# Kernel tuning notes

Measured on AMD Instinct MI355X. Metric: run time of the kernel, lower is better.

The kernel has to match this reference:

```python
import jax, jax.numpy as jnp
import numpy as np

B, N, D, H = 4, 4096, 1024, 16
HD = D // H  # 64
EPS_NORM = 1e-12  # F.normalize eps
EPS_LN = 1e-5     # layernorm eps


def setup_inputs() -> dict:
    key = jax.random.key(0)
    ks = jax.random.split(key, 9)
    s = 0.02
    return {
        "x": jax.random.normal(ks[0], (B, N, D), jnp.float32),
        "Wq": jax.random.normal(ks[1], (D, D), jnp.float32) * s,
        "Wk": jax.random.normal(ks[2], (D, D), jnp.float32) * s,
        "Wv": jax.random.normal(ks[3], (D, D), jnp.float32) * s,
        "Wf": jax.random.normal(ks[4], (H, D), jnp.float32) * s,
        "Wg1": jax.random.normal(ks[5], (HD, D), jnp.float32) * s,
        "Wg2": jax.random.normal(ks[6], (D, HD), jnp.float32) * s,
        "ln_w": jnp.ones((D,), jnp.float32),
        "Wo": jax.random.normal(ks[7], (D, D), jnp.float32) * s,
    }


def _silu(x):
    return x * jax.nn.sigmoid(x)


def _simple_gla(q, k, v, f):
    # q,k,v: [B,N,H,HD], f: [B,N,H] log-decay. Recurrence:
    #   S_t = exp(f_t) * S_{t-1} + k_t v_t^T ;  o_t = q_t^T S_t  (scale=1)
    qT = jnp.moveaxis(q, 1, 0)  # [N,B,H,HD]
    kT = jnp.moveaxis(k, 1, 0)
    vT = jnp.moveaxis(v, 1, 0)
    fT = jnp.moveaxis(f, 1, 0)  # [N,B,H]

    def step(S, inp):
        qt, kt, vt, ft = inp
        S = jnp.exp(ft)[..., None, None] * S + kt[..., :, None] * vt[..., None, :]
        o = jnp.einsum('bhk,bhkv->bhv', qt, S)
        return S, o

    S0 = jnp.zeros((q.shape[0], q.shape[2], q.shape[3], v.shape[3]), q.dtype)
    _, o = jax.lax.scan(step, S0, (qT, kT, vT, fT))
    return jnp.moveaxis(o, 0, 1)  # [B,N,H,HD]


def reference(x, Wq, Wk, Wv, Wf, Wg1, Wg2, ln_w, Wo):
    b, n, d = x.shape
    q = _silu(x @ Wq.T).reshape(b, n, H, HD)
    k = _silu(x @ Wk.T).reshape(b, n, H, HD)
    v = _silu(x @ Wv.T).reshape(b, n, H, HD)
    f = jax.nn.log_sigmoid(x @ Wf.T)  # [B,N,H] scalar per-head log decay
    # F.normalize(k, p=2, dim=-1)
    k = k / jnp.maximum(jnp.linalg.norm(k, axis=-1, keepdims=True), EPS_NORM)

    o = _simple_gla(q, k, v, f).reshape(b, n, d)

    # output gate: sigmoid(Linear(d->hd) -> Linear(hd->d))
    gate = jax.nn.sigmoid((x @ Wg1.T) @ Wg2.T)
    o = o * gate

    # layernorm without bias
    mu = jnp.mean(o, axis=-1, keepdims=True)
    xc = o - mu
    var = jnp.mean(xc * xc, axis=-1, keepdims=True)
    o = xc / jnp.sqrt(var + EPS_LN) * ln_w

    return o @ Wo.T
```

## Files before the change

kernel.cpp:

```cpp
#include <hip/hip_runtime.h>
#include <stdint.h>


#define NWIDE 3200

typedef __attribute__((ext_vector_type(4))) float f32x4;
typedef __attribute__((ext_vector_type(4))) unsigned short u16x4;
typedef __attribute__((ext_vector_type(8))) unsigned short u16x8;
typedef __attribute__((ext_vector_type(8))) __bf16 bf16x8;

__device__ __forceinline__ float bf2f(unsigned short u) {
    union { unsigned int i; float f; } c; c.i = ((unsigned int)u) << 16; return c.f;
}
__device__ __forceinline__ unsigned short f2bf(float f) {
    union { float f; unsigned int i; } c; c.f = f;
    return (unsigned short)((c.i + 0x7fffu + ((c.i >> 16) & 1u)) >> 16);
}
__device__ __forceinline__ float siluf(float x) { return x / (1.f + __expf(-x)); }
__device__ __forceinline__ float logsigf(float z) {
    return (z >= 0.f) ? -log1pf(__expf(-z)) : (z - log1pf(__expf(z)));
}
__device__ __forceinline__ f32x4 MFMA(bf16x8 a, bf16x8 b, f32x4 c) {
    return __builtin_amdgcn_mfma_f32_16x16x32_bf16(a, b, c, 0, 0, 0);
}
__device__ __forceinline__ void lds16(const void* g, void* l) {
    __builtin_amdgcn_global_load_lds(
        (const __attribute__((address_space(1))) unsigned int*)(uintptr_t)g,
        (__attribute__((address_space(3))) unsigned int*)(unsigned int)(uintptr_t)l,
        16, 0, 0);
}

__global__ __launch_bounds__(256)
void k_prep(const float* __restrict__ x, const float* __restrict__ Wq, const float* __restrict__ Wk,
            const float* __restrict__ Wv, const float* __restrict__ Wf, const float* __restrict__ Wg1,
            const float* __restrict__ Wg2, const float* __restrict__ lnw, const float* __restrict__ Wo,
            unsigned short* __restrict__ xb, unsigned short* __restrict__ Wcat,
            unsigned short* __restrict__ Wob, unsigned short* __restrict__ Wg2b,
            float* __restrict__ scol) {
    const int blk = blockIdx.x, t = threadIdx.x;
    if (blk < 16384) {
        const int i = blk * 256 + t;
        f32x4 v = ((const f32x4*)x)[i];
        u16x4 o;
#pragma unroll
        for (int e = 0; e < 4; e++) o[e] = f2bf(v[e]);
        ((u16x4*)xb)[i] = o;
    } else if (blk < 19584) {
        const int r = blk - 16384;
        const float* src = nullptr; int sr = r;
        if (r < 1024) { src = Wq; }
        else if (r < 2048) { src = Wk; sr = r - 1024; }
        else if (r < 3072) { src = Wv; sr = r - 2048; }
        else if (r < 3088) { src = Wf; sr = r - 3072; }
        else if (r < 3152) { src = Wg1; sr = r - 3088; }
        u16x4 o;
        if (src) {
            f32x4 v = *(const f32x4*)&src[(size_t)sr * 1024 + 4 * t];
#pragma unroll
            for (int e = 0; e < 4; e++) o[e] = f2bf(v[e]);
        } else {
            o[0] = 0; o[1] = 0; o[2] = 0; o[3] = 0;
        }
        *(u16x4*)&Wcat[(size_t)r * 1024 + 4 * t] = o;
    } else if (blk < 20608) {
        __shared__ float red[4];
        const int c = blk - 19584;
        f32x4 wv = *(const f32x4*)&Wo[(size_t)c * 1024 + 4 * t];
        f32x4 lv = *(const f32x4*)&lnw[4 * t];
        u16x4 o; float ps = 0.f;
#pragma unroll
        for (int e = 0; e < 4; e++) { o[e] = f2bf(wv[e] * lv[e]); ps += bf2f(o[e]); }
        *(u16x4*)&Wob[(size_t)c * 1024 + 4 * t] = o;
#pragma unroll
        for (int m = 1; m < 64; m <<= 1) ps += __shfl_xor(ps, m, 64);
        if ((t & 63) == 0) red[t >> 6] = ps;
        __syncthreads();
        if (t == 0) scol[c] = red[0] + red[1] + red[2] + red[3];
    } else {
        const int i = (blk - 20608) * 256 + t;
        f32x4 v = ((const f32x4*)Wg2)[i];
        u16x4 o;
#pragma unroll
        for (int e = 0; e < 4; e++) o[e] = f2bf(v[e]);
        ((u16x4*)Wg2b)[i] = o;
    }
}

template <int MODE>
__global__ __launch_bounds__(256)
void k_gemm(const unsigned short* __restrict__ A, const unsigned short* __restrict__ Bw,
            void* __restrict__ outp, float* __restrict__ zbuf,
            const float* __restrict__ stats, const float* __restrict__ scol,
            int M, int N, int K, int ldOut) {
    __shared__ __align__(16) unsigned short As[128 * 64];
    __shared__ __align__(16) unsigned short Bs[128 * 64];
    const int tid = threadIdx.x;
    const int w = tid >> 6, lane = tid & 63;
    const int m0 = blockIdx.x * 128, n0 = blockIdx.y * 128;
    const int fr = lane & 15, fg = lane >> 4;
    const int wr = w >> 1, wc = w & 1;
    const int srow = lane >> 3;
    const int schunk = (lane & 7) ^ (srow & 7);
    f32x4 acc[4][4] = {};
    const int kc = K >> 6;
    for (int kt = 0; kt < kc; ++kt) {
        const int k0 = kt << 6;
        __syncthreads();
#pragma unroll
        for (int q = 0; q < 4; q++) {
            const int rr = 32 * w + 8 * q;
            lds16(A + (size_t)(m0 + rr + srow) * K + k0 + schunk * 8, &As[rr * 64]);
            lds16(Bw + (size_t)(n0 + rr + srow) * K + k0 + schunk * 8, &Bs[rr * 64]);
        }
        __syncthreads();
        bf16x8 av[4][2], bv[4][2];
#pragma unroll
        for (int i = 0; i < 4; i++)
#pragma unroll
            for (int ks = 0; ks < 2; ks++) {
                const int row = 64 * wr + 16 * i + fr;
                av[i][ks] = *(const bf16x8*)&As[row * 64 + (((ks * 4 + fg) ^ (row & 7)) << 3)];
            }
#pragma unroll
        for (int j = 0; j < 4; j++)
#pragma unroll
            for (int ks = 0; ks < 2; ks++) {
                const int row = 64 * wc + 16 * j + fr;
                bv[j][ks] = *(const bf16x8*)&Bs[row * 64 + (((ks * 4 + fg) ^ (row & 7)) << 3)];
            }
#pragma unroll
        for (int i = 0; i < 4; i++)
#pragma unroll
            for (int j = 0; j < 4; j++)
#pragma unroll
                for (int ks = 0; ks < 2; ks++)
                    acc[i][j] = MFMA(av[i][ks], bv[j][ks], acc[i][j]);
    }
    const int nb = n0 + 64 * wc;
    if (MODE == 1) {
        float* O = (float*)outp;
        float sj[4];
#pragma unroll
        for (int j = 0; j < 4; j++) sj[j] = scol[nb + 16 * j + fr];
#pragma unroll
        for (int i = 0; i < 4; i++)
#pragma unroll
            for (int r = 0; r < 4; r++) {
                const int gr = m0 + 64 * wr + 16 * i + 4 * fg + r;
                const float mu = stats[gr * 2], rs = stats[gr * 2 + 1];
#pragma unroll
                for (int j = 0; j < 4; j++)
                    O[(size_t)gr * ldOut + nb + 16 * j + fr] = rs * (acc[i][j][r] - mu * sj[j]);
            }
        return;
    }
    unsigned short* Y = (unsigned short*)outp;
    if (nb >= 3072) {
#pragma unroll
        for (int i = 0; i < 4; i++)
#pragma unroll
            for (int j = 0; j < 4; j++) {
                const int gc = nb + 16 * j + fr;
#pragma unroll
                for (int r = 0; r < 4; r++) {
                    const int gr = m0 + 64 * wr + 16 * i + 4 * fg + r;
                    const float v = acc[i][j][r];
                    if (gc < 3088) {
                        if (gc >= 3072) zbuf[gr * 16 + (gc - 3072)] = v;
                    } else if (gc < 3152) {
                        Y[(size_t)gr * ldOut + gc] = f2bf(v);
                    }
                }
            }
    } else {
#pragma unroll
        for (int i = 0; i < 4; i++)
#pragma unroll
            for (int j = 0; j < 4; j++) {
                const int gc = nb + 16 * j + fr;
#pragma unroll
                for (int r = 0; r < 4; r++)
                    Y[(size_t)(m0 + 64 * wr + 16 * i + 4 * fg + r) * ldOut + gc] = f2bf(acc[i][j][r]);
            }
    }
}

__global__ __launch_bounds__(256)
void k_chunk_kv(const unsigned short* __restrict__ Y, const float* __restrict__ zbuf,
                float* __restrict__ cbuf, unsigned short* __restrict__ St) {
    __shared__ __align__(16) unsigned short Kt[64 * 72];
    __shared__ __align__(16) unsigned short Vt[64 * 72];
    __shared__ float cs[64];
    const int cid = blockIdx.x, tid = threadIdx.x;
    const int bh = cid >> 6, ic = cid & 63;
    const int b = bh >> 4, h = bh & 15;
    if (tid < 64) {
        float v = logsigf(zbuf[(size_t)(b * 4096 + ic * 64 + tid) * 16 + h]);
#pragma unroll
        for (int off = 1; off < 64; off <<= 1) {
            float u = __shfl_up(v, (unsigned)off, 64);
            if (tid >= off) v += u;
        }
        cs[tid] = v;
        cbuf[(size_t)cid * 64 + tid] = v;
    }
    __syncthreads();
    const int s = tid >> 2, c0 = (tid & 3) << 4;
    const float wdec = __expf(cs[63] - cs[s]);
    const size_t rowg = (size_t)(b * 4096 + ic * 64 + s) * NWIDE;
    u16x8 k0v = *(const u16x8*)&Y[rowg + 1024 + h * 64 + c0];
    u16x8 k1v = *(const u16x8*)&Y[rowg + 1024 + h * 64 + c0 + 8];
    u16x8 v0v = *(const u16x8*)&Y[rowg + 2048 + h * 64 + c0];
    u16x8 v1v = *(const u16x8*)&Y[rowg + 2048 + h * 64 + c0 + 8];
    float kf[16]; float ss = 0.f;
#pragma unroll
    for (int e = 0; e < 8; e++) { kf[e] = siluf(bf2f(k0v[e])); ss += kf[e] * kf[e]; }
#pragma unroll
    for (int e = 0; e < 8; e++) { kf[8 + e] = siluf(bf2f(k1v[e])); ss += kf[8 + e] * kf[8 + e]; }
    ss += __shfl_xor(ss, 1, 64);
    ss += __shfl_xor(ss, 2, 64);
    const float sc = wdec / fmaxf(sqrtf(ss), 1e-12f);
#pragma unroll
    for (int e = 0; e < 8; e++) {
        Kt[(c0 + e) * 72 + s] = f2bf(kf[e] * sc);
        Kt[(c0 + 8 + e) * 72 + s] = f2bf(kf[8 + e] * sc);
        Vt[(c0 + e) * 72 + s] = f2bf(siluf(bf2f(v0v[e])));
        Vt[(c0 + 8 + e) * 72 + s] = f2bf(siluf(bf2f(v1v[e])));
    }
    __syncthreads();
    const int w = tid >> 6, lane = tid & 63;
    const int fr = lane & 15, fg = lane >> 4;
    f32x4 acc[4] = {};
#pragma unroll
    for (int ks = 0; ks < 2; ks++) {
        bf16x8 a = *(const bf16x8*)&Kt[(16 * w + fr) * 72 + ks * 32 + fg * 8];
#pragma unroll
        for (int j = 0; j < 4; j++)
            acc[j] = MFMA(a, *(const bf16x8*)&Vt[(16 * j + fr) * 72 + ks * 32 + fg * 8], acc[j]);
    }
    unsigned short* outp = St + (size_t)cid * 4096;
#pragma unroll
    for (int j = 0; j < 4; j++)
#pragma unroll
        for (int r = 0; r < 4; r++)
            outp[(16 * w + 4 * fg + r) * 64 + 16 * j + fr] = f2bf(acc[j][r]);
}

__global__ void k_scan(unsigned short* __restrict__ St, const float* __restrict__ cbuf) {
    const int bh = blockIdx.x >> 4;
    const int e = ((blockIdx.x & 15) << 8) + threadIdx.x;
    float S = 0.f;
    const size_t base = (size_t)bh * 64 * 4096 + e;
    for (int i = 0; i < 64; i++) {
        const float d = __expf(cbuf[(bh * 64 + i) * 64 + 63]);
        const float m = bf2f(St[base + (size_t)i * 4096]);
        St[base + (size_t)i * 4096] = f2bf(S);
        S = d * S + m;
    }
}

__global__ __launch_bounds__(256)
void k_chunk_out(const unsigned short* __restrict__ Y, const float* __restrict__ cbuf,
                 const unsigned short* __restrict__ St, const unsigned short* __restrict__ Wg2b,
                 unsigned short* __restrict__ og) {
    __shared__ __align__(16) unsigned short Qs[64 * 72];
    __shared__ __align__(16) unsigned short Ks[64 * 72];
    __shared__ __align__(16) unsigned short Vt[64 * 72];
    __shared__ __align__(16) unsigned short S0[64 * 72];
    __shared__ __align__(16) unsigned short G1[64 * 72];
    __shared__ __align__(16) unsigned short W2[64 * 72];
    __shared__ __align__(16) unsigned short Pl[4 * 16 * 72];
    __shared__ float cs[64];
    const int cid = blockIdx.x, tid = threadIdx.x;
    const int bh = cid >> 6, ic = cid & 63;
    const int b = bh >> 4, h = bh & 15;
    if (tid < 64) cs[tid] = cbuf[(size_t)cid * 64 + tid];
    const int s = tid >> 2, c0 = (tid & 3) << 4;
    const size_t rowg = (size_t)(b * 4096 + ic * 64 + s) * NWIDE;
    {
        u16x8 q0 = *(const u16x8*)&Y[rowg + h * 64 + c0];
        u16x8 q1 = *(const u16x8*)&Y[rowg + h * 64 + c0 + 8];
        u16x8 o0, o1;
#pragma unroll
        for (int e = 0; e < 8; e++) { o0[e] = f2bf(siluf(bf2f(q0[e]))); o1[e] = f2bf(siluf(bf2f(q1[e]))); }
        *(u16x8*)&Qs[s * 72 + c0] = o0;
        *(u16x8*)&Qs[s * 72 + c0 + 8] = o1;
    }
    {
        u16x8 k0v = *(const u16x8*)&Y[rowg + 1024 + h * 64 + c0];
        u16x8 k1v = *(const u16x8*)&Y[rowg + 1024 + h * 64 + c0 + 8];
        float kf[16]; float ssn = 0.f;
#pragma unroll
        for (int e = 0; e < 8; e++) { kf[e] = siluf(bf2f(k0v[e])); ssn += kf[e] * kf[e]; }
#pragma unroll
        for (int e = 0; e < 8; e++) { kf[8 + e] = siluf(bf2f(k1v[e])); ssn += kf[8 + e] * kf[8 + e]; }
        ssn += __shfl_xor(ssn, 1, 64);
        ssn += __shfl_xor(ssn, 2, 64);
        const float scn = 1.f / fmaxf(sqrtf(ssn), 1e-12f);
        u16x8 o0, o1;
#pragma unroll
        for (int e = 0; e < 8; e++) { o0[e] = f2bf(kf[e] * scn); o1[e] = f2bf(kf[8 + e] * scn); }
        *(u16x8*)&Ks[s * 72 + c0] = o0;
        *(u16x8*)&Ks[s * 72 + c0 + 8] = o1;
    }
    *(u16x8*)&G1[s * 72 + c0] = *(const u16x8*)&Y[rowg + 3088 + c0];
    *(u16x8*)&G1[s * 72 + c0 + 8] = *(const u16x8*)&Y[rowg + 3088 + c0 + 8];
    *(u16x8*)&W2[s * 72 + c0] = *(const u16x8*)&Wg2b[(size_t)(h * 64 + s) * 64 + c0];
    *(u16x8*)&W2[s * 72 + c0 + 8] = *(const u16x8*)&Wg2b[(size_t)(h * 64 + s) * 64 + c0 + 8];
    {
        u16x8 v0v = *(const u16x8*)&Y[rowg + 2048 + h * 64 + c0];
        u16x8 v1v = *(const u16x8*)&Y[rowg + 2048 + h * 64 + c0 + 8];
        u16x8 s0v = *(const u16x8*)&St[(size_t)cid * 4096 + s * 64 + c0];
        u16x8 s1v = *(const u16x8*)&St[(size_t)cid * 4096 + s * 64 + c0 + 8];
#pragma unroll
        for (int e = 0; e < 8; e++) {
            Vt[(c0 + e) * 72 + s] = f2bf(siluf(bf2f(v0v[e])));
            Vt[(c0 + 8 + e) * 72 + s] = f2bf(siluf(bf2f(v1v[e])));
            S0[(c0 + e) * 72 + s] = s0v[e];
            S0[(c0 + 8 + e) * 72 + s] = s1v[e];
        }
    }
    __syncthreads();
    const int w = tid >> 6, lane = tid & 63;
    const int fr = lane & 15, fg = lane >> 4;
    bf16x8 aq[2];
#pragma unroll
    for (int ks = 0; ks < 2; ks++) aq[ks] = *(const bf16x8*)&Qs[(16 * w + fr) * 72 + ks * 32 + fg * 8];
    f32x4 sc[4] = {};
#pragma unroll
    for (int ks = 0; ks < 2; ks++)
#pragma unroll
        for (int j = 0; j < 4; j++)
            sc[j] = MFMA(aq[ks], *(const bf16x8*)&Ks[(16 * j + fr) * 72 + ks * 32 + fg * 8], sc[j]);
    const int tl = 16 * w + 4 * fg;
#pragma unroll
    for (int j = 0; j < 4; j++)
#pragma unroll
        for (int r = 0; r < 4; r++) {
            const int tt = tl + r, ss2 = 16 * j + fr;
            float p = (ss2 <= tt) ? sc[j][r] * __expf(cs[tt] - cs[ss2]) : 0.f;
            Pl[w * (16 * 72) + (4 * fg + r) * 72 + ss2] = f2bf(p);
        }
    __syncthreads();
    f32x4 ov[4] = {};
#pragma unroll
    for (int ks = 0; ks < 2; ks++) {
        bf16x8 ap = *(const bf16x8*)&Pl[w * (16 * 72) + fr * 72 + ks * 32 + fg * 8];
#pragma unroll
        for (int j = 0; j < 4; j++)
            ov[j] = MFMA(ap, *(const bf16x8*)&Vt[(16 * j + fr) * 72 + ks * 32 + fg * 8], ov[j]);
    }
    f32x4 qs[4] = {};
#pragma unroll
    for (int ks = 0; ks < 2; ks++)
#pragma unroll
        for (int j = 0; j < 4; j++)
            qs[j] = MFMA(aq[ks], *(const bf16x8*)&S0[(16 * j + fr) * 72 + ks * 32 + fg * 8], qs[j]);
    bf16x8 ag[2];
#pragma unroll
    for (int ks = 0; ks < 2; ks++) ag[ks] = *(const bf16x8*)&G1[(16 * w + fr) * 72 + ks * 32 + fg * 8];
    f32x4 gl[4] = {};
#pragma unroll
    for (int ks = 0; ks < 2; ks++)
#pragma unroll
        for (int j = 0; j < 4; j++)
            gl[j] = MFMA(ag[ks], *(const bf16x8*)&W2[(16 * j + fr) * 72 + ks * 32 + fg * 8], gl[j]);
#pragma unroll
    for (int j = 0; j < 4; j++)
#pragma unroll
        for (int r = 0; r < 4; r++) {
            const int tt = tl + r;
            const float o = ov[j][r] + __expf(cs[tt]) * qs[j][r];
            const float g = 1.f / (1.f + __expf(-gl[j][r]));
            og[(size_t)(b * 4096 + ic * 64 + tt) * 1024 + h * 64 + 16 * j + fr] = f2bf(o * g);
        }
}

__global__ __launch_bounds__(256)
void k_lnstats(const unsigned short* __restrict__ og, float* __restrict__ stats) {
    const int row = blockIdx.x * 4 + (threadIdx.x >> 6);
    const int lane = threadIdx.x & 63;
    const unsigned short* p = og + (size_t)row * 1024 + lane * 16;
    u16x8 a = *(const u16x8*)p;
    u16x8 b2 = *(const u16x8*)(p + 8);
    float s = 0.f, q = 0.f;
#pragma unroll
    for (int e = 0; e < 8; e++) { float x = bf2f(a[e]); s += x; q += x * x; }
#pragma unroll
    for (int e = 0; e < 8; e++) { float x = bf2f(b2[e]); s += x; q += x * x; }
#pragma unroll
    for (int m = 1; m < 64; m <<= 1) { s += __shfl_xor(s, m, 64); q += __shfl_xor(q, m, 64); }
    if (lane == 0) {
        const float mu = s * (1.f / 1024.f);
        const float var = q * (1.f / 1024.f) - mu * mu;
        stats[row * 2] = mu;
        stats[row * 2 + 1] = rsqrtf(var + 1e-5f);
    }
}

extern "C" void kernel_launch(void* const* d_in, const int* in_sizes, int n_in,
                              void* d_out, int out_size, void* d_ws, size_t ws_size,
                              hipStream_t stream) {
    const float* x = (const float*)d_in[0];
    const float* Wq = (const float*)d_in[1];
    const float* Wk = (const float*)d_in[2];
    const float* Wv = (const float*)d_in[3];
    const float* Wf = (const float*)d_in[4];
    const float* Wg1 = (const float*)d_in[5];
    const float* Wg2 = (const float*)d_in[6];
    const float* lnw = (const float*)d_in[7];
    const float* Wo = (const float*)d_in[8];
    char* ws = (char*)d_ws;
    unsigned short* xb = (unsigned short*)(ws + 0);
    unsigned short* Yb = (unsigned short*)(ws + 33554432LL);
    unsigned short* Wcat = (unsigned short*)(ws + 138412032LL);
    unsigned short* Wob = (unsigned short*)(ws + 144965632LL);
    unsigned short* Wg2b = (unsigned short*)(ws + 147062784LL);
    float* zbuf = (float*)(ws + 147193856LL);
    float* cbuf = (float*)(ws + 148242432LL);
    unsigned short* St = (unsigned short*)(ws + 149291008LL);
    float* scol = (float*)(ws + 182845440LL);
    float* stats = (float*)(ws + 182849536LL);
    unsigned short* og = xb;

    k_prep<<<20672, 256, 0, stream>>>(x, Wq, Wk, Wv, Wf, Wg1, Wg2, lnw, Wo,
                                      xb, Wcat, Wob, Wg2b, scol);
    k_gemm<0><<<dim3(128, 25), 256, 0, stream>>>(xb, Wcat, Yb, zbuf, nullptr, nullptr,
                                                 16384, 3200, 1024, 3200);
    k_chunk_kv<<<4096, 256, 0, stream>>>(Yb, zbuf, cbuf, St);
    k_scan<<<1024, 256, 0, stream>>>(St, cbuf);
    k_chunk_out<<<4096, 256, 0, stream>>>(Yb, cbuf, St, Wg2b, og);
    k_lnstats<<<4096, 256, 0, stream>>>(og, stats);
    k_gemm<1><<<dim3(128, 8), 256, 0, stream>>>(og, Wob, d_out, nullptr, stats, scol,
                                                16384, 1024, 1024, 1024);
}
```

Baseline: 334.6 us.

## Triple-buffer GEMM LDS loads, swap grid order, and vectorize chunk scan

The bf16 GEMM now uses a three-stage LDS ring with BK=32: it prefetches two k-tiles ahead via global_load_lds and waits with explicit vmcnt plus a raw barrier in place of a double __syncthreads per iteration. It uses inline ds_read_b128, a new XOR swizzle, and s_setprio around the MFMA block. The grid is transposed so consecutive blocks walk along N and share the same A rows. Separately, the inter-chunk scan handles four elements per thread with 8-byte loads and stores on a quarter of the blocks. Risks are in the hand-written waitcnt accounting and the smaller K step per barrier.

```diff
diff --git a/kernel.cpp b/kernel.cpp
--- a/kernel.cpp
+++ b/kernel.cpp
@@ -5,6 +5,7 @@
 #define NWIDE 3200
 
 typedef __attribute__((ext_vector_type(4))) float f32x4;
+typedef __attribute__((ext_vector_type(4))) unsigned int u32x4;
 typedef __attribute__((ext_vector_type(4))) unsigned short u16x4;
 typedef __attribute__((ext_vector_type(8))) unsigned short u16x8;
 typedef __attribute__((ext_vector_type(8))) __bf16 bf16x8;
@@ -29,6 +30,12 @@
         (__attribute__((address_space(3))) unsigned int*)(unsigned int)(uintptr_t)l,
         16, 0, 0);
 }
+__device__ __forceinline__ bf16x8 lds_rd16(unsigned addr) {
+    u32x4 r;
+    asm volatile("ds_read_b128 %0, %1" : "=v"(r) : "v"(addr));
+    return __builtin_bit_cast(bf16x8, r);
+}
+#define GBAR() do { asm volatile("" ::: "memory"); __builtin_amdgcn_s_barrier(); asm volatile("" ::: "memory"); } while (0)
 
 __global__ __launch_bounds__(256)
 void k_prep(const float* __restrict__ x, const float* __restrict__ Wq, const float* __restrict__ Wk,
@@ -86,56 +93,70 @@
     }
 }
 
-template <int MODE>
+template <int MODE, int NK>
 __global__ __launch_bounds__(256)
 void k_gemm(const unsigned short* __restrict__ A, const unsigned short* __restrict__ Bw,
             void* __restrict__ outp, float* __restrict__ zbuf,
-            const float* __restrict__ stats, const float* __restrict__ scol,
-            int M, int N, int K, int ldOut) {
-    __shared__ __align__(16) unsigned short As[128 * 64];
-    __shared__ __align__(16) unsigned short Bs[128 * 64];
+            const float* __restrict__ stats, const float* __restrict__ scol, int ldOut) {
+    __shared__ __align__(16) char smem[49152];
+    const unsigned lbase = (unsigned)(uintptr_t)&smem[0];
     const int tid = threadIdx.x;
     const int w = tid >> 6, lane = tid & 63;
-    const int m0 = blockIdx.x * 128, n0 = blockIdx.y * 128;
     const int fr = lane & 15, fg = lane >> 4;
     const int wr = w >> 1, wc = w & 1;
-    const int srow = lane >> 3;
-    const int schunk = (lane & 7) ^ (srow & 7);
+    const int m0 = blockIdx.y * 128, n0 = blockIdx.x * 128;
+    const int kc = NK >> 5;
+
+    auto STAGE = [&](int kt, int buf) {
+        const int k0 = kt << 5;
+        char* dbase = smem + buf * 16384;
+#pragma unroll
+        for (int q = 0; q < 2; q++) {
+            const int slot = (q << 8) + tid;
+            const int r = slot >> 2, c = slot & 3;
+            const int gc8 = (c ^ (r & 3) ^ ((r >> 2) & 3)) << 3;
+            char* dst = dbase + (((q << 8) + (w << 6)) << 4);
+            lds16(A + (size_t)(m0 + r) * NK + k0 + gc8, dst);
+            lds16(Bw + (size_t)(n0 + r) * NK + k0 + gc8, dst + 8192);
+        }
+    };
+
     f32x4 acc[4][4] = {};
-    const int kc = K >> 6;
-    for (int kt = 0; kt < kc; ++kt) {
-        const int k0 = kt << 6;
-        __syncthreads();
-#pragma unroll
-        for (int q = 0; q < 4; q++) {
-            const int rr = 32 * w + 8 * q;
-            lds16(A + (size_t)(m0 + rr + srow) * K + k0 + schunk * 8, &As[rr * 64]);
-            lds16(Bw + (size_t)(n0 + rr + srow) * K + k0 + schunk * 8, &Bs[rr * 64]);
-        }
-        __syncthreads();
-        bf16x8 av[4][2], bv[4][2];
+
+    STAGE(0, 0); STAGE(1, 1);
+    asm volatile("s_waitcnt vmcnt(4)" ::: "memory");
+    GBAR();
+
+    int cb = 0;
+    for (int t = 0; t < kc; ++t) {
+        const int sb = (cb >= 1) ? cb - 1 : 2;
+        if (t + 2 < kc) STAGE(t + 2, sb);
+        const unsigned boff = (unsigned)(cb * 16384);
+        bf16x8 av[4], bv[4];
+#pragma unroll
+        for (int i = 0; i < 4; i++) {
+            const int rowA = 64 * wr + 16 * i + fr;
+            av[i] = lds_rd16(lbase + boff + rowA * 64 +
+                             ((fg ^ (rowA & 3) ^ ((rowA >> 2) & 3)) << 4));
+            const int rowB = 64 * wc + 16 * i + fr;
+            bv[i] = lds_rd16(lbase + boff + 8192 + rowB * 64 +
+                             ((fg ^ (rowB & 3) ^ ((rowB >> 2) & 3)) << 4));
+        }
+        asm volatile("s_waitcnt lgkmcnt(0)" ::: "memory");
+        __builtin_amdgcn_sched_barrier(0);
+        __builtin_amdgcn_s_setprio(1);
 #pragma unroll
         for (int i = 0; i < 4; i++)
 #pragma unroll
-            for (int ks = 0; ks < 2; ks++) {
-                const int row = 64 * wr + 16 * i + fr;
-                av[i][ks] = *(const bf16x8*)&As[row * 64 + (((ks * 4 + fg) ^ (row & 7)) << 3)];
-            }
-#pragma unroll
-        for (int j = 0; j < 4; j++)
-#pragma unroll
-            for (int ks = 0; ks < 2; ks++) {
-                const int row = 64 * wc + 16 * j + fr;
-                bv[j][ks] = *(const bf16x8*)&Bs[row * 64 + (((ks * 4 + fg) ^ (row & 7)) << 3)];
-            }
-#pragma unroll
-        for (int i = 0; i < 4; i++)
-#pragma unroll
             for (int j = 0; j < 4; j++)
-#pragma unroll
-                for (int ks = 0; ks < 2; ks++)
-                    acc[i][j] = MFMA(av[i][ks], bv[j][ks], acc[i][j]);
-    }
+                acc[i][j] = MFMA(av[i], bv[j], acc[i][j]);
+        __builtin_amdgcn_s_setprio(0);
+        if (t + 2 < kc) asm volatile("s_waitcnt vmcnt(4)" ::: "memory");
+        else            asm volatile("s_waitcnt vmcnt(0)" ::: "memory");
+        GBAR();
+        cb = (cb == 2) ? 0 : cb + 1;
+    }
+
     const int nb = n0 + 64 * wc;
     if (MODE == 1) {
         float* O = (float*)outp;
@@ -246,16 +267,19 @@
             outp[(16 * w + 4 * fg + r) * 64 + 16 * j + fr] = f2bf(acc[j][r]);
 }
 
-__global__ void k_scan(unsigned short* __restrict__ St, const float* __restrict__ cbuf) {
-    const int bh = blockIdx.x >> 4;
-    const int e = ((blockIdx.x & 15) << 8) + threadIdx.x;
-    float S = 0.f;
-    const size_t base = (size_t)bh * 64 * 4096 + e;
+__global__ __launch_bounds__(256)
+void k_scan(unsigned short* __restrict__ St, const float* __restrict__ cbuf) {
+    const int bh = blockIdx.x >> 2;
+    const int e0 = (((blockIdx.x & 3) << 8) + threadIdx.x) << 2;
+    float S[4] = {0.f, 0.f, 0.f, 0.f};
+    const size_t base = (size_t)bh * 64 * 4096 + e0;
     for (int i = 0; i < 64; i++) {
         const float d = __expf(cbuf[(bh * 64 + i) * 64 + 63]);
-        const float m = bf2f(St[base + (size_t)i * 4096]);
-        St[base + (size_t)i * 4096] = f2bf(S);
-        S = d * S + m;
+        u16x4 m = *(u16x4*)&St[base + (size_t)i * 4096];
+        u16x4 o;
+#pragma unroll
+        for (int e = 0; e < 4; e++) { o[e] = f2bf(S[e]); S[e] = d * S[e] + bf2f(m[e]); }
+        *(u16x4*)&St[base + (size_t)i * 4096] = o;
     }
 }
 
@@ -425,12 +449,10 @@
 
     k_prep<<<20672, 256, 0, stream>>>(x, Wq, Wk, Wv, Wf, Wg1, Wg2, lnw, Wo,
                                       xb, Wcat, Wob, Wg2b, scol);
-    k_gemm<0><<<dim3(128, 25), 256, 0, stream>>>(xb, Wcat, Yb, zbuf, nullptr, nullptr,
-                                                 16384, 3200, 1024, 3200);
+    k_gemm<0, 1024><<<dim3(25, 128), 256, 0, stream>>>(xb, Wcat, Yb, zbuf, nullptr, nullptr, 3200);
     k_chunk_kv<<<4096, 256, 0, stream>>>(Yb, zbuf, cbuf, St);
-    k_scan<<<1024, 256, 0, stream>>>(St, cbuf);
+    k_scan<<<256, 256, 0, stream>>>(St, cbuf);
     k_chunk_out<<<4096, 256, 0, stream>>>(Yb, cbuf, St, Wg2b, og);
     k_lnstats<<<4096, 256, 0, stream>>>(og, stats);
-    k_gemm<1><<<dim3(128, 8), 256, 0, stream>>>(og, Wob, d_out, nullptr, stats, scol,
-                                                16384, 1024, 1024, 1024);
-}
+    k_gemm<1, 1024><<<dim3(8, 128), 256, 0, stream>>>(og, Wob, d_out, nullptr, stats, scol, 1024);
+}
```

New measurement: 347.7 us. +3.9%, slower.
